# Kernel optimization log

Hardware: AMD Instinct MI355X
Metric: run time of the kernel (lower is better)

The kernel has to match this reference:

```python
import math
import jax, jax.numpy as jnp
import numpy as np

EMBED_DIM = 768
NUM_HEADS = 12
SCALE = 0.125
KERNEL_SIZE = 5
SIGMA = 1.0


def gaussian_kernel1d(ksize, sigma):
    x = jnp.arange(ksize, dtype=jnp.float32) - (ksize - 1) / 2.0
    g = jnp.exp(-0.5 * (x / sigma) ** 2)
    return g / g.sum()


def gaussian_blur_2d(x, ksize, sigma):
    # x: [N, C, P, P]; per-channel (depthwise) separable gaussian blur,
    # reflect padding, matching torchvision.transforms.functional.gaussian_blur.
    N, C, P, _ = x.shape
    g = gaussian_kernel1d(ksize, sigma)
    k2d = jnp.outer(g, g)[None, None]  # [1,1,k,k] (separable == full outer kernel)
    pad = ksize // 2
    xp = jnp.pad(x.reshape(N * C, 1, P, P), ((0, 0), (0, 0), (pad, pad), (pad, pad)), mode='reflect')
    y = jax.lax.conv_general_dilated(
        xp, k2d.astype(x.dtype), window_strides=(1, 1), padding='VALID',
        dimension_numbers=('NCHW', 'OIHW', 'NCHW'))
    return y.reshape(N, C, P, P)


def setup_inputs() -> dict:
    key = jax.random.key(0)
    k1, k2 = jax.random.split(key)
    B, S, E = 8, 1024, EMBED_DIM
    x = jax.random.normal(k1, (B, S, E), dtype=jnp.float32)
    # xavier_uniform for [3E, E]
    bound = math.sqrt(6.0 / (3 * E + E))
    W_in = jax.random.uniform(k2, (3 * E, E), dtype=jnp.float32, minval=-bound, maxval=bound)
    return {"x": x, "W_in": W_in}


def reference(x, W_in):
    B, S, E = x.shape
    H, D = NUM_HEADS, E // NUM_HEADS
    # fused QKV projection; chunk order is (values, keys, queries)
    qkv = jnp.einsum('bse,fe->bsf', x, W_in)  # [B, S, 3E]
    _v, k, q = jnp.split(qkv, 3, axis=-1)

    def to_heads(t):
        return t.reshape(B, S, H, D).transpose(0, 2, 1, 3).reshape(B * H, S, D)

    q, k = to_heads(q), to_heads(k)
    logits = SCALE * jnp.einsum('nqd,nkd->nqk', q, k)  # [B*H, S, S]
    P = int(math.sqrt(S))
    logits4 = logits.reshape(B * H, S, P, P)  # key axis viewed as PxP patch grid
    blurred = gaussian_blur_2d(logits4, KERNEL_SIZE, SIGMA)
    attn = jax.nn.softmax(blurred.reshape(B * H, S, S), axis=-1)
    return attn
```

## Files before the change

### kernel.cpp

```cpp
#include <hip/hip_runtime.h>


typedef __attribute__((ext_vector_type(8))) short short8;
typedef __attribute__((ext_vector_type(4))) float f32x4;

__device__ __forceinline__ float bf2f(unsigned short u) {
    unsigned int v = ((unsigned int)u) << 16;
    return __builtin_bit_cast(float, v);
}
__device__ __forceinline__ unsigned short f2bf(float f) {
    unsigned int u = __builtin_bit_cast(unsigned int, f);
    u += 0x7FFFu + ((u >> 16) & 1u);
    return (unsigned short)(u >> 16);
}

__device__ __forceinline__ void g2lds16(const unsigned short* g, unsigned short* l) {
    __builtin_amdgcn_global_load_lds(
        (const __attribute__((address_space(1))) void*)g,
        (__attribute__((address_space(3))) void*)l, 16, 0, 0);
}

#if defined(__has_builtin) && __has_builtin(__builtin_amdgcn_exp2f)
#define EXP2F(x) __builtin_amdgcn_exp2f(x)
#else
#define EXP2F(x) exp2f(x)
#endif

#define QSCALE 0.1803368801111204f

__global__ __launch_bounds__(256) void k_cast(const float* __restrict__ x,
                                              const float* __restrict__ w,
                                              unsigned short* __restrict__ dst) {
    const int NX = 8 * 1024 * 768;
    int i = (blockIdx.x * 256 + threadIdx.x) * 4;
    float4 v;
    if (i < NX) v = *(const float4*)(x + i);
    else        v = *(const float4*)(w + 768 * 768 + (i - NX));
    ushort4 o;
    o.x = f2bf(v.x); o.y = f2bf(v.y); o.z = f2bf(v.z); o.w = f2bf(v.w);
    *(ushort4*)(dst + i) = o;
}

__global__ __launch_bounds__(256) void k_proj(const unsigned short* __restrict__ xb,
                                              const unsigned short* __restrict__ wb,
                                              unsigned short* __restrict__ qh,
                                              unsigned short* __restrict__ kh) {
    __shared__ unsigned short As[128 * 64];
    __shared__ unsigned short Bs[128 * 64];

    const int lane = threadIdx.x & 63;
    const int wv   = threadIdx.x >> 6;
    const int m0   = blockIdx.x * 128;
    const int n0   = blockIdx.y * 128;
    const int col  = lane & 15;
    const int quad = lane >> 4;
    const int wm   = (wv >> 1) * 64;
    const int wn   = (wv & 1) * 64;

    const int srow   = wv * 32 + (lane >> 3);
    const int schunk = ((lane & 7) ^ ((lane >> 3) & 7)) * 8;
    const unsigned short* ag = xb + (size_t)(m0 + srow) * 768 + schunk;
    const unsigned short* bg = wb + (size_t)(n0 + srow) * 768 + schunk;
    unsigned short* al = As + (wv * 32) * 64;
    unsigned short* bl = Bs + (wv * 32) * 64;

    f32x4 acc[4][4] = {};

    for (int kk = 0; kk < 768; kk += 64) {
        __syncthreads();
#pragma unroll
        for (int j = 0; j < 4; ++j) {
            g2lds16(ag + j * 8 * 768 + kk, al + j * 8 * 64);
            g2lds16(bg + j * 8 * 768 + kk, bl + j * 8 * 64);
        }
        __syncthreads();

#pragma unroll
        for (int kc = 0; kc < 2; ++kc) {
            const int ch = ((kc * 4 + quad) ^ (col & 7)) * 8;
            short8 a[4], b[4];
#pragma unroll
            for (int mt = 0; mt < 4; ++mt)
                a[mt] = *(const short8*)(const void*)(As + (wm + mt * 16 + col) * 64 + ch);
#pragma unroll
            for (int nt = 0; nt < 4; ++nt)
                b[nt] = *(const short8*)(const void*)(Bs + (wn + nt * 16 + col) * 64 + ch);
#pragma unroll
            for (int mt = 0; mt < 4; ++mt)
#pragma unroll
                for (int nt = 0; nt < 4; ++nt)
                    acc[mt][nt] = __builtin_amdgcn_mfma_f32_16x16x32_bf16(
                        a[mt], b[nt], acc[mt][nt], 0, 0, 0);
        }
    }

#pragma unroll
    for (int nt = 0; nt < 4; ++nt) {
        int f = n0 + wn + nt * 16 + col;
        bool isq = (f >= 768);
        int fl = isq ? (f - 768) : f;
        int h = fl >> 6, d = fl & 63;
        unsigned short* dstb = isq ? qh : kh;
        float scl = isq ? QSCALE : 1.0f;
#pragma unroll
        for (int mt = 0; mt < 4; ++mt) {
#pragma unroll
            for (int i = 0; i < 4; ++i) {
                int t = m0 + wm + mt * 16 + quad * 4 + i;
                int n = (t >> 10) * 12 + h;
                dstb[((n << 10) + (t & 1023)) * 64 + d] = f2bf(acc[mt][nt][i] * scl);
            }
        }
    }
}

template <int VERT>
__global__ __launch_bounds__(256) void k_blur(const unsigned short* __restrict__ src,
                                              unsigned short* __restrict__ dst) {
    int t  = blockIdx.x * 256 + threadIdx.x;
    int dq = t & 15;
    int sk = (t >> 4) & 1023;
    int n  = t >> 14;
    int r = sk >> 5, c = sk & 31;
    const float g[5] = {0.054488684f, 0.24420134f, 0.40261995f, 0.24420134f, 0.054488684f};
    float acc0 = 0.f, acc1 = 0.f, acc2 = 0.f, acc3 = 0.f;
#pragma unroll
    for (int o = -2; o <= 2; ++o) {
        int p = (VERT ? r : c) + o;
        if (p < 0)  p = -p;
        if (p > 31) p = 62 - p;
        int sk2 = VERT ? (p * 32 + c) : (r * 32 + p);
        const unsigned short* sp = src + ((n << 10) + sk2) * 64 + dq * 4;
        uint2 u = *(const uint2*)(const void*)sp;
        float w = g[o + 2];
        acc0 += w * bf2f((unsigned short)(u.x & 0xffff));
        acc1 += w * bf2f((unsigned short)(u.x >> 16));
        acc2 += w * bf2f((unsigned short)(u.y & 0xffff));
        acc3 += w * bf2f((unsigned short)(u.y >> 16));
    }
    uint2 ov;
    ov.x = (unsigned)f2bf(acc0) | ((unsigned)f2bf(acc1) << 16);
    ov.y = (unsigned)f2bf(acc2) | ((unsigned)f2bf(acc3) << 16);
    *(uint2*)(void*)(dst + ((n << 10) + sk) * 64 + dq * 4) = ov;
}

__global__ __launch_bounds__(256) void k_attn(const unsigned short* __restrict__ qh,
                                              const unsigned short* __restrict__ kt,
                                              float* __restrict__ out) {
    const int lane = threadIdx.x & 63;
    const int wv   = threadIdx.x >> 6;
    const int n    = blockIdx.y;
    const int s0   = blockIdx.x * 16;
    const int col  = lane & 15;
    const int kq   = (lane >> 4) * 8;

    __shared__ float red[2][4][16];

    const unsigned short* qp = qh + ((n << 10) + s0 + col) * 64 + kq;
    short8 a0 = *(const short8*)(const void*)(qp);
    short8 a1 = *(const short8*)(const void*)(qp + 32);

    f32x4 acc[16];
    const unsigned short* kp = kt + ((n << 10) + wv * 256 + col) * 64 + kq;
#pragma unroll
    for (int t = 0; t < 16; ++t) {
        short8 b0 = *(const short8*)(const void*)(kp + t * 1024);
        short8 b1 = *(const short8*)(const void*)(kp + t * 1024 + 32);
        f32x4 c = {};
        c = __builtin_amdgcn_mfma_f32_16x16x32_bf16(a0, b0, c, 0, 0, 0);
        c = __builtin_amdgcn_mfma_f32_16x16x32_bf16(a1, b1, c, 0, 0, 0);
        acc[t] = c;
    }

    float mx[4];
#pragma unroll
    for (int i = 0; i < 4; ++i) {
        float m = acc[0][i];
#pragma unroll
        for (int t = 1; t < 16; ++t) m = fmaxf(m, acc[t][i]);
#pragma unroll
        for (int off = 1; off < 16; off <<= 1) m = fmaxf(m, __shfl_xor(m, off, 64));
        mx[i] = m;
    }
    if (col == 0) {
#pragma unroll
        for (int i = 0; i < 4; ++i) red[0][wv][(lane >> 4) * 4 + i] = mx[i];
    }
    __syncthreads();

    float sm[4];
#pragma unroll
    for (int i = 0; i < 4; ++i) {
        int qloc = (lane >> 4) * 4 + i;
        float m = fmaxf(fmaxf(red[0][0][qloc], red[0][1][qloc]),
                        fmaxf(red[0][2][qloc], red[0][3][qloc]));
        float s = 0.f;
#pragma unroll
        for (int t = 0; t < 16; ++t) {
            float e = EXP2F(acc[t][i] - m);
            acc[t][i] = e;
            s += e;
        }
#pragma unroll
        for (int off = 1; off < 16; off <<= 1) s += __shfl_xor(s, off, 64);
        sm[i] = s;
    }
    if (col == 0) {
#pragma unroll
        for (int i = 0; i < 4; ++i) red[1][wv][(lane >> 4) * 4 + i] = sm[i];
    }
    __syncthreads();

#pragma unroll
    for (int i = 0; i < 4; ++i) {
        int qloc = (lane >> 4) * 4 + i;
        float s = red[1][0][qloc] + red[1][1][qloc] + red[1][2][qloc] + red[1][3][qloc];
        float inv = 1.0f / s;
        float* op = out + (((size_t)(n << 10) + s0 + qloc) << 10) + wv * 256 + col;
#pragma unroll
        for (int t = 0; t < 16; ++t) op[t * 16] = acc[t][i] * inv;
    }
}

extern "C" void kernel_launch(void* const* d_in, const int* in_sizes, int n_in,
                              void* d_out, int out_size, void* d_ws, size_t ws_size,
                              hipStream_t stream) {
    const float* x = (const float*)d_in[0];
    const float* W = (const float*)d_in[1];
    float* out = (float*)d_out;

    unsigned short* ws   = (unsigned short*)d_ws;
    unsigned short* xb   = ws;
    unsigned short* wb   = xb + 6291456;
    unsigned short* qh   = wb + 1179648;
    unsigned short* kh   = qh + 6291456;
    unsigned short* ktmp = kh + 6291456;
    unsigned short* kt   = ktmp + 6291456;

    k_cast<<<7296, 256, 0, stream>>>(x, W, xb);
    k_proj<<<dim3(64, 12), 256, 0, stream>>>(xb, wb, qh, kh);
    k_blur<1><<<6144, 256, 0, stream>>>(kh, ktmp);
    k_blur<0><<<6144, 256, 0, stream>>>(ktmp, kt);
    k_attn<<<dim3(64, 96), 256, 0, stream>>>(qh, kt, out);
}
```

Baseline: 535.8 us.

## Fuse separable blur passes via LDS and transpose MFMA for vectorized softmax stores

The two separate vertical and horizontal blur kernels become one kernel. It stages a 1024x16 slice of keys in LDS, does both passes there, and drops the intermediate global buffer and one launch. In the attention kernel the MFMA operands are swapped so each lane holds four consecutive key columns for one query row. This lets the row max and sum reductions use fewer shuffles and makes the output writes 16-byte nontemporal vector stores instead of scattered scalar stores. The blur kernel's grid is small (384 blocks) and it uses 64KB of LDS per block, which limits occupancy.

```diff
diff --git a/kernel.cpp b/kernel.cpp
--- a/kernel.cpp
+++ b/kernel.cpp
@@ -114,34 +114,72 @@
     }
 }
 
-template <int VERT>
-__global__ __launch_bounds__(256) void k_blur(const unsigned short* __restrict__ src,
-                                              unsigned short* __restrict__ dst) {
-    int t  = blockIdx.x * 256 + threadIdx.x;
-    int dq = t & 15;
-    int sk = (t >> 4) & 1023;
-    int n  = t >> 14;
-    int r = sk >> 5, c = sk & 31;
+__global__ __launch_bounds__(256) void k_blur2(const unsigned short* __restrict__ src,
+                                               unsigned short* __restrict__ dst) {
+    __shared__ unsigned short sb[1024 * 16];
+    __shared__ unsigned short tb[1024 * 16];
+
+    const int t  = threadIdx.x;
+    const int n  = blockIdx.y;
+    const int dc = blockIdx.x * 16;
+    const int c4 = (t & 3) * 4;
+    const int k0 = t >> 2;
     const float g[5] = {0.054488684f, 0.24420134f, 0.40261995f, 0.24420134f, 0.054488684f};
-    float acc0 = 0.f, acc1 = 0.f, acc2 = 0.f, acc3 = 0.f;
-#pragma unroll
-    for (int o = -2; o <= 2; ++o) {
-        int p = (VERT ? r : c) + o;
-        if (p < 0)  p = -p;
-        if (p > 31) p = 62 - p;
-        int sk2 = VERT ? (p * 32 + c) : (r * 32 + p);
-        const unsigned short* sp = src + ((n << 10) + sk2) * 64 + dq * 4;
-        uint2 u = *(const uint2*)(const void*)sp;
-        float w = g[o + 2];
-        acc0 += w * bf2f((unsigned short)(u.x & 0xffff));
-        acc1 += w * bf2f((unsigned short)(u.x >> 16));
-        acc2 += w * bf2f((unsigned short)(u.y & 0xffff));
-        acc3 += w * bf2f((unsigned short)(u.y >> 16));
-    }
-    uint2 ov;
-    ov.x = (unsigned)f2bf(acc0) | ((unsigned)f2bf(acc1) << 16);
-    ov.y = (unsigned)f2bf(acc2) | ((unsigned)f2bf(acc3) << 16);
-    *(uint2*)(void*)(dst + ((n << 10) + sk) * 64 + dq * 4) = ov;
+
+    const unsigned short* gp = src + (((size_t)n << 10) + k0) * 64 + dc + c4;
+#pragma unroll
+    for (int it = 0; it < 16; ++it)
+        *(uint2*)(void*)(sb + ((it * 64 + k0) << 4) + c4) =
+            *(const uint2*)(const void*)(gp + (size_t)it * 64 * 64);
+    __syncthreads();
+
+#pragma unroll
+    for (int it = 0; it < 16; ++it) {
+        int key = it * 64 + k0;
+        int r = key >> 5, c = key & 31;
+        float a0 = 0.f, a1 = 0.f, a2 = 0.f, a3 = 0.f;
+#pragma unroll
+        for (int o = -2; o <= 2; ++o) {
+            int p = r + o;
+            if (p < 0)  p = -p;
+            if (p > 31) p = 62 - p;
+            uint2 u = *(const uint2*)(const void*)(sb + (((p << 5) + c) << 4) + c4);
+            float w = g[o + 2];
+            a0 += w * bf2f((unsigned short)(u.x & 0xffff));
+            a1 += w * bf2f((unsigned short)(u.x >> 16));
+            a2 += w * bf2f((unsigned short)(u.y & 0xffff));
+            a3 += w * bf2f((unsigned short)(u.y >> 16));
+        }
+        uint2 ov;
+        ov.x = (unsigned)f2bf(a0) | ((unsigned)f2bf(a1) << 16);
+        ov.y = (unsigned)f2bf(a2) | ((unsigned)f2bf(a3) << 16);
+        *(uint2*)(void*)(tb + (key << 4) + c4) = ov;
+    }
+    __syncthreads();
+
+    unsigned short* op = dst + (((size_t)n << 10) + k0) * 64 + dc + c4;
+#pragma unroll
+    for (int it = 0; it < 16; ++it) {
+        int key = it * 64 + k0;
+        int rb = key & ~31, c = key & 31;
+        float a0 = 0.f, a1 = 0.f, a2 = 0.f, a3 = 0.f;
+#pragma unroll
+        for (int o = -2; o <= 2; ++o) {
+            int p = c + o;
+            if (p < 0)  p = -p;
+            if (p > 31) p = 62 - p;
+            uint2 u = *(const uint2*)(const void*)(tb + ((rb + p) << 4) + c4);
+            float w = g[o + 2];
+            a0 += w * bf2f((unsigned short)(u.x & 0xffff));
+            a1 += w * bf2f((unsigned short)(u.x >> 16));
+            a2 += w * bf2f((unsigned short)(u.y & 0xffff));
+            a3 += w * bf2f((unsigned short)(u.y >> 16));
+        }
+        uint2 ov;
+        ov.x = (unsigned)f2bf(a0) | ((unsigned)f2bf(a1) << 16);
+        ov.y = (unsigned)f2bf(a2) | ((unsigned)f2bf(a3) << 16);
+        *(uint2*)(void*)(op + (size_t)it * 64 * 64) = ov;
+    }
 }
 
 __global__ __launch_bounds__(256) void k_attn(const unsigned short* __restrict__ qh,
@@ -152,73 +190,70 @@
     const int n    = blockIdx.y;
     const int s0   = blockIdx.x * 16;
     const int col  = lane & 15;
-    const int kq   = (lane >> 4) * 8;
+    const int quad = lane >> 4;
+    const int kq   = quad * 8;
 
     __shared__ float red[2][4][16];
 
-    const unsigned short* qp = qh + ((n << 10) + s0 + col) * 64 + kq;
-    short8 a0 = *(const short8*)(const void*)(qp);
-    short8 a1 = *(const short8*)(const void*)(qp + 32);
+    const unsigned short* qp = qh + (((size_t)n << 10) + s0 + col) * 64 + kq;
+    short8 q0 = *(const short8*)(const void*)(qp);
+    short8 q1 = *(const short8*)(const void*)(qp + 32);
 
     f32x4 acc[16];
-    const unsigned short* kp = kt + ((n << 10) + wv * 256 + col) * 64 + kq;
+    const unsigned short* kp = kt + (((size_t)n << 10) + wv * 256 + col) * 64 + kq;
 #pragma unroll
     for (int t = 0; t < 16; ++t) {
         short8 b0 = *(const short8*)(const void*)(kp + t * 1024);
         short8 b1 = *(const short8*)(const void*)(kp + t * 1024 + 32);
         f32x4 c = {};
-        c = __builtin_amdgcn_mfma_f32_16x16x32_bf16(a0, b0, c, 0, 0, 0);
-        c = __builtin_amdgcn_mfma_f32_16x16x32_bf16(a1, b1, c, 0, 0, 0);
+        c = __builtin_amdgcn_mfma_f32_16x16x32_bf16(b0, q0, c, 0, 0, 0);
+        c = __builtin_amdgcn_mfma_f32_16x16x32_bf16(b1, q1, c, 0, 0, 0);
         acc[t] = c;
     }
 
-    float mx[4];
-#pragma unroll
-    for (int i = 0; i < 4; ++i) {
-        float m = acc[0][i];
-#pragma unroll
-        for (int t = 1; t < 16; ++t) m = fmaxf(m, acc[t][i]);
-#pragma unroll
-        for (int off = 1; off < 16; off <<= 1) m = fmaxf(m, __shfl_xor(m, off, 64));
-        mx[i] = m;
-    }
-    if (col == 0) {
-#pragma unroll
-        for (int i = 0; i < 4; ++i) red[0][wv][(lane >> 4) * 4 + i] = mx[i];
-    }
-    __syncthreads();
-
-    float sm[4];
-#pragma unroll
-    for (int i = 0; i < 4; ++i) {
-        int qloc = (lane >> 4) * 4 + i;
-        float m = fmaxf(fmaxf(red[0][0][qloc], red[0][1][qloc]),
-                        fmaxf(red[0][2][qloc], red[0][3][qloc]));
-        float s = 0.f;
-#pragma unroll
-        for (int t = 0; t < 16; ++t) {
+    float m;
+    {
+        float mt[16];
+#pragma unroll
+        for (int t = 0; t < 16; ++t)
+            mt[t] = fmaxf(fmaxf(acc[t][0], acc[t][1]), fmaxf(acc[t][2], acc[t][3]));
+#pragma unroll
+        for (int off = 8; off >= 1; off >>= 1)
+#pragma unroll
+            for (int t2 = 0; t2 < off; ++t2) mt[t2] = fmaxf(mt[t2], mt[t2 + off]);
+        m = mt[0];
+        m = fmaxf(m, __shfl_xor(m, 16, 64));
+        m = fmaxf(m, __shfl_xor(m, 32, 64));
+    }
+    if (quad == 0) red[0][wv][col] = m;
+    __syncthreads();
+
+    m = fmaxf(fmaxf(red[0][0][col], red[0][1][col]),
+              fmaxf(red[0][2][col], red[0][3][col]));
+
+    float s = 0.f;
+#pragma unroll
+    for (int t = 0; t < 16; ++t) {
+#pragma unroll
+        for (int i = 0; i < 4; ++i) {
             float e = EXP2F(acc[t][i] - m);
             acc[t][i] = e;
             s += e;
         }
-#pragma unroll
-        for (int off = 1; off < 16; off <<= 1) s += __shfl_xor(s, off, 64);
-        sm[i] = s;
-    }
-    if (col == 0) {
-#pragma unroll
-        for (int i = 0; i < 4; ++i) red[1][wv][(lane >> 4) * 4 + i] = sm[i];
-    }
-    __syncthreads();
-
-#pragma unroll
-    for (int i = 0; i < 4; ++i) {
-        int qloc = (lane >> 4) * 4 + i;
-        float s = red[1][0][qloc] + red[1][1][qloc] + red[1][2][qloc] + red[1][3][qloc];
-        float inv = 1.0f / s;
-        float* op = out + (((size_t)(n << 10) + s0 + qloc) << 10) + wv * 256 + col;
-#pragma unroll
-        for (int t = 0; t < 16; ++t) op[t * 16] = acc[t][i] * inv;
+    }
+    s += __shfl_xor(s, 16, 64);
+    s += __shfl_xor(s, 32, 64);
+    if (quad == 0) red[1][wv][col] = s;
+    __syncthreads();
+
+    s = red[1][0][col] + red[1][1][col] + red[1][2][col] + red[1][3][col];
+    float inv = 1.0f / s;
+
+    f32x4* op = (f32x4*)(out + ((((size_t)n << 10) + s0 + col) << 10) + wv * 256 + quad * 4);
+#pragma unroll
+    for (int t = 0; t < 16; ++t) {
+        f32x4 v = acc[t] * inv;
+        __builtin_nontemporal_store(v, op + t * 4);
     }
 }
 
@@ -234,12 +269,10 @@
     unsigned short* wb   = xb + 6291456;
     unsigned short* qh   = wb + 1179648;
     unsigned short* kh   = qh + 6291456;
-    unsigned short* ktmp = kh + 6291456;
-    unsigned short* kt   = ktmp + 6291456;
+    unsigned short* kt   = kh + 6291456;
 
     k_cast<<<7296, 256, 0, stream>>>(x, W, xb);
     k_proj<<<dim3(64, 12), 256, 0, stream>>>(xb, wb, qh, kh);
-    k_blur<1><<<6144, 256, 0, stream>>>(kh, ktmp);
-    k_blur<0><<<6144, 256, 0, stream>>>(ktmp, kt);
+    k_blur2<<<dim3(4, 96), 256, 0, stream>>>(kh, kt);
     k_attn<<<dim3(64, 96), 256, 0, stream>>>(qh, kt, out);
 }
```

After: 554.9 us. 3.6% more time.
